# Kernel optimization log

Hardware: AMD Instinct MI355X
Metric: run time of the kernel (lower is better)

## Reference

```python
import jax, jax.numpy as jnp
import numpy as np

H, W = 1024, 1024
NUM_FEATURES = 64
NUM_PILLARS = 100000


def setup_inputs() -> dict:
    key = jax.random.key(0)
    k1, k2 = jax.random.split(key)
    pillar_features = jax.random.normal(k1, (NUM_PILLARS, NUM_FEATURES), dtype=jnp.float32)
    coords = jax.random.randint(k2, (NUM_PILLARS, 3), 0, 1024, dtype=jnp.int64)
    return {"pillar_features": pillar_features, "coords": coords}


def reference(pillar_features, coords):
    # pillar_features: [N, F]; coords: [N, 3] = (batch_idx, y_idx, x_idx)
    x_idx = coords[:, 2]
    y_idx = coords[:, 1]
    valid = (x_idx >= 0) & (x_idx < W) & (y_idx >= 0) & (y_idx < H)
    # Flatten spatial dims; route invalid pillars to an out-of-bounds slot
    # that mode='drop' discards (matches the torch valid_mask filtering).
    flat_idx = jnp.where(valid, y_idx * W + x_idx, H * W)
    img = jnp.zeros((NUM_FEATURES, H * W), dtype=pillar_features.dtype)
    # single vectorized scatter: [F, N] updates into [F, H*W]
    img = img.at[:, flat_idx].set(pillar_features.T, mode='drop')
    return img.reshape(1, NUM_FEATURES, H, W)
```

## Files before the change

kernel.cpp:

```cpp
#include <hip/hip_runtime.h>


constexpr int H  = 1024;
constexpr int W  = 1024;
constexpr int HW = H * W;
constexpr int NF = 64;

__global__ void winner_kernel(const int* __restrict__ coords,
                              int* __restrict__ winner, int np) {
    int p = blockIdx.x * blockDim.x + threadIdx.x;
    if (p >= np) return;
    int y = coords[p * 3 + 1];
    int x = coords[p * 3 + 2];
    if ((unsigned)x < (unsigned)W && (unsigned)y < (unsigned)H) {
        atomicMax(winner + (y * W + x), p);
    }
}

__global__ void __launch_bounds__(256) fill_kernel(const float* __restrict__ feat,
                                                   const int* __restrict__ winner,
                                                   float* __restrict__ out) {
    int g    = blockIdx.x * blockDim.x + threadIdx.x;
    int cell = g * 4;

    int4 w = *(const int4*)(winner + cell);
    const float* r0 = feat + (size_t)max(w.x, 0) * NF;
    const float* r1 = feat + (size_t)max(w.y, 0) * NF;
    const float* r2 = feat + (size_t)max(w.z, 0) * NF;
    const float* r3 = feat + (size_t)max(w.w, 0) * NF;
    bool v0 = w.x >= 0, v1 = w.y >= 0, v2 = w.z >= 0, v3 = w.w >= 0;

    float* o = out + cell;
#pragma unroll 4
    for (int f = 0; f < NF; ++f) {
        float4 v;
        v.x = v0 ? r0[f] : 0.0f;
        v.y = v1 ? r1[f] : 0.0f;
        v.z = v2 ? r2[f] : 0.0f;
        v.w = v3 ? r3[f] : 0.0f;
        *(float4*)(o + (size_t)f * HW) = v;
    }
}

extern "C" void kernel_launch(void* const* d_in, const int* in_sizes, int n_in,
                              void* d_out, int out_size, void* d_ws, size_t ws_size,
                              hipStream_t stream) {
    const float* feat   = (const float*)d_in[0];
    const int*   coords = (const int*)d_in[1];
    float*       out    = (float*)d_out;
    int np = in_sizes[1] / 3;

    int* winner = (int*)d_ws;

    hipMemsetAsync(winner, 0xFF, (size_t)HW * sizeof(int), stream);

    winner_kernel<<<(np + 255) / 256, 256, 0, stream>>>(coords, winner, np);

    fill_kernel<<<HW / 4 / 256, 256, 0, stream>>>(feat, winner, out);
}
```

Baseline: 310.4 us.

## Stage pillar feature rows through LDS to transpose gather into coalesced stores

The fill kernel now handles a tile of 64 cells per block. It loads each winning pillar's feature row into shared memory with coalesced float4 reads, then transposes through padded LDS so each feature plane is written with float4 stores. This replaces the old pattern of strided scalar reads across four rows per thread. The cost is two block barriers, LDS traffic, and many more, smaller blocks. The output write of roughly 256MB still dominates, so the possible gain is limited.

Result: no change. 306.9 us (-1.1%).

```diff
diff --git a/kernel.cpp b/kernel.cpp
--- a/kernel.cpp
+++ b/kernel.cpp
@@ -5,6 +5,8 @@
 constexpr int W  = 1024;
 constexpr int HW = H * W;
 constexpr int NF = 64;
+constexpr int TILE = 64;
+constexpr int LSTR = NF + 1;
 
 __global__ void winner_kernel(const int* __restrict__ coords,
                               int* __restrict__ winner, int np) {
@@ -20,25 +22,47 @@
 __global__ void __launch_bounds__(256) fill_kernel(const float* __restrict__ feat,
                                                    const int* __restrict__ winner,
                                                    float* __restrict__ out) {
-    int g    = blockIdx.x * blockDim.x + threadIdx.x;
-    int cell = g * 4;
+    __shared__ float lds[TILE * LSTR];
+    __shared__ int   wc[TILE];
 
-    int4 w = *(const int4*)(winner + cell);
-    const float* r0 = feat + (size_t)max(w.x, 0) * NF;
-    const float* r1 = feat + (size_t)max(w.y, 0) * NF;
-    const float* r2 = feat + (size_t)max(w.z, 0) * NF;
-    const float* r3 = feat + (size_t)max(w.w, 0) * NF;
-    bool v0 = w.x >= 0, v1 = w.y >= 0, v2 = w.z >= 0, v3 = w.w >= 0;
+    const int base = blockIdx.x * TILE;
+    const int t    = threadIdx.x;
 
-    float* o = out + cell;
-#pragma unroll 4
-    for (int f = 0; f < NF; ++f) {
-        float4 v;
-        v.x = v0 ? r0[f] : 0.0f;
-        v.y = v1 ? r1[f] : 0.0f;
-        v.z = v2 ? r2[f] : 0.0f;
-        v.w = v3 ? r3[f] : 0.0f;
-        *(float4*)(o + (size_t)f * HW) = v;
+    if (t < TILE) wc[t] = winner[base + t];
+    __syncthreads();
+
+    {
+        const int c  = t >> 2;
+        const int j  = t & 3;
+        const int wp = wc[c];
+        float* dst = lds + c * LSTR + j * 16;
+        if (wp >= 0) {
+            const float4* row = (const float4*)(feat + (size_t)wp * NF) + j * 4;
+            float4 a = row[0], b = row[1], cc = row[2], d = row[3];
+            dst[0]=a.x; dst[1]=a.y; dst[2]=a.z; dst[3]=a.w;
+            dst[4]=b.x; dst[5]=b.y; dst[6]=b.z; dst[7]=b.w;
+            dst[8]=cc.x; dst[9]=cc.y; dst[10]=cc.z; dst[11]=cc.w;
+            dst[12]=d.x; dst[13]=d.y; dst[14]=d.z; dst[15]=d.w;
+        } else {
+#pragma unroll
+            for (int k = 0; k < 16; ++k) dst[k] = 0.0f;
+        }
+    }
+    __syncthreads();
+
+    {
+        const int f0 = t >> 4;
+        const int cg = t & 15;
+#pragma unroll
+        for (int iter = 0; iter < 4; ++iter) {
+            const int f = iter * 16 + f0;
+            float4 v;
+            v.x = lds[(cg * 4 + 0) * LSTR + f];
+            v.y = lds[(cg * 4 + 1) * LSTR + f];
+            v.z = lds[(cg * 4 + 2) * LSTR + f];
+            v.w = lds[(cg * 4 + 3) * LSTR + f];
+            *(float4*)(out + (size_t)f * HW + base + cg * 4) = v;
+        }
     }
 }
 
@@ -53,8 +77,6 @@
     int* winner = (int*)d_ws;
 
     hipMemsetAsync(winner, 0xFF, (size_t)HW * sizeof(int), stream);
-
     winner_kernel<<<(np + 255) / 256, 256, 0, stream>>>(coords, winner, np);
-
-    fill_kernel<<<HW / 4 / 256, 256, 0, stream>>>(feat, winner, out);
+    fill_kernel<<<HW / TILE, 256, 0, stream>>>(feat, winner, out);
 }
```

## Restructure fill kernel so each block handles one feature over a cell span

Applied to the files above, without the earlier changes.

Each fill block now owns one feature channel and a contiguous span of 16384 cells, so a block's writes all land in one feature plane. Before, each thread wrote four cells across all 64 feature planes. The change trades write locality for re-reading the winner array 64 times, once per feature, and for strided single-float gathers from the feature rows. The intent is to improve write streaming and DRAM page locality, at the cost of more total winner traffic and less reuse of each feature row across features.

Result: slower. 361.1 us (+16.3%).

```diff
diff --git a/kernel.cpp b/kernel.cpp
--- a/kernel.cpp
+++ b/kernel.cpp
@@ -1,10 +1,11 @@
 #include <hip/hip_runtime.h>
 
 
-constexpr int H  = 1024;
-constexpr int W  = 1024;
-constexpr int HW = H * W;
-constexpr int NF = 64;
+constexpr int H    = 1024;
+constexpr int W    = 1024;
+constexpr int HW   = H * W;
+constexpr int NF   = 64;
+constexpr int SPAN = 16384;
 
 __global__ void winner_kernel(const int* __restrict__ coords,
                               int* __restrict__ winner, int np) {
@@ -20,25 +21,25 @@
 __global__ void __launch_bounds__(256) fill_kernel(const float* __restrict__ feat,
                                                    const int* __restrict__ winner,
                                                    float* __restrict__ out) {
-    int g    = blockIdx.x * blockDim.x + threadIdx.x;
-    int cell = g * 4;
+    const int bid = blockIdx.x;
+    const int f   = bid & 63;
+    const int s   = bid >> 6;
+    const int c0  = s * SPAN;
+    const int t   = threadIdx.x;
 
-    int4 w = *(const int4*)(winner + cell);
-    const float* r0 = feat + (size_t)max(w.x, 0) * NF;
-    const float* r1 = feat + (size_t)max(w.y, 0) * NF;
-    const float* r2 = feat + (size_t)max(w.z, 0) * NF;
-    const float* r3 = feat + (size_t)max(w.w, 0) * NF;
-    bool v0 = w.x >= 0, v1 = w.y >= 0, v2 = w.z >= 0, v3 = w.w >= 0;
+    const int*   wbase = winner + c0;
+    float*       obase = out + (size_t)f * HW + c0;
 
-    float* o = out + cell;
 #pragma unroll 4
-    for (int f = 0; f < NF; ++f) {
+    for (int i = 0; i < SPAN / 1024; ++i) {
+        const int c = i * 1024 + t * 4;
+        int4 w = *(const int4*)(wbase + c);
         float4 v;
-        v.x = v0 ? r0[f] : 0.0f;
-        v.y = v1 ? r1[f] : 0.0f;
-        v.z = v2 ? r2[f] : 0.0f;
-        v.w = v3 ? r3[f] : 0.0f;
-        *(float4*)(o + (size_t)f * HW) = v;
+        v.x = (w.x >= 0) ? feat[(size_t)w.x * NF + f] : 0.0f;
+        v.y = (w.y >= 0) ? feat[(size_t)w.y * NF + f] : 0.0f;
+        v.z = (w.z >= 0) ? feat[(size_t)w.z * NF + f] : 0.0f;
+        v.w = (w.w >= 0) ? feat[(size_t)w.w * NF + f] : 0.0f;
+        *(float4*)(obase + c) = v;
     }
 }
 
@@ -52,9 +53,7 @@
 
     int* winner = (int*)d_ws;
 
-    hipMemsetAsync(winner, 0xFF, (size_t)HW * sizeof(int), stream);
-
+    (void)hipMemsetAsync(winner, 0xFF, (size_t)HW * sizeof(int), stream);
     winner_kernel<<<(np + 255) / 256, 256, 0, stream>>>(coords, winner, np);
-
-    fill_kernel<<<HW / 4 / 256, 256, 0, stream>>>(feat, winner, out);
+    fill_kernel<<<NF * (HW / SPAN), 256, 0, stream>>>(feat, winner, out);
 }
```
